# Kernel optimization log

Hardware: AMD Instinct MI355X
Metric: run time of the kernel (lower is better)

Reference implementation:

```python
import jax, jax.numpy as jnp
import numpy as np

DIM = 512
H = 8
HD = DIM // H
MAXREL = 8
BF16_MIN = -3.3895313892515355e38  # torch.finfo(torch.bfloat16).min


def setup_inputs() -> dict:
    key = jax.random.key(0)
    k1, k2, k3, k4, k5, k6 = jax.random.split(key, 6)
    b, l, n, d = 4, 16, 64, DIM
    x = jax.random.normal(k1, (b, l, n, d), dtype=jnp.float32)
    time_embeddings = jax.random.normal(k2, (b, l, d), dtype=jnp.float32)
    # relative frame positions in [-MAXREL, MAXREL]
    pos = jax.random.randint(k3, (b, l, l), 0, 2 * MAXREL + 1) - MAXREL
    pos = pos.astype(jnp.int64) if jax.config.read('jax_enable_x64') else pos.astype(jnp.int32)
    # causal mask over frames
    mask = jnp.tril(jnp.ones((l, l), dtype=jnp.int32))[None].repeat(b, axis=0)
    # params (torch Linear convention: out = x @ W.T)
    W_qkv = jax.random.normal(k4, (3 * d, d), dtype=jnp.float32) * (1.0 / np.sqrt(d))
    W_tqkv = jax.random.normal(k5, (3 * HD, d), dtype=jnp.float32) * (1.0 / np.sqrt(d))
    # xavier_uniform for embeddings table [2*max+1, head_dim]
    lim = np.sqrt(6.0 / (2 * MAXREL + 1 + HD))
    emb_table = jax.random.uniform(k6, (2 * MAXREL + 1, HD), minval=-lim, maxval=lim, dtype=jnp.float32)
    return {"x": x, "time_embeddings": time_embeddings, "pos": pos, "mask": mask,
            "W_qkv": W_qkv, "W_tqkv": W_tqkv, "emb_table": emb_table}


def _forward(x, time_embeddings, pos, mask, W_qkv, W_tqkv, emb_table):
    b, l, n, d = x.shape
    h, hd = H, HD
    N = l * n
    scale = np.sqrt(d).astype(np.float32)

    qkv = jnp.einsum('blnd,ed->blne', x, W_qkv)
    q, k, v = jnp.split(qkv, 3, axis=-1)

    def to_heads(t):  # [b,l,n,d] -> [b,h,l,n,hd]
        return t.reshape(b, l, n, h, hd).transpose(0, 3, 1, 2, 4)
    q, k, v = to_heads(q), to_heads(k), to_heads(v)

    # time qkv: [b,l,3*hd] -> broadcast add over heads and tokens
    tqkv = jnp.einsum('bld,ed->ble', time_embeddings, W_tqkv)
    qt, kt, vt = jnp.split(tqkv, 3, axis=-1)  # each [b,l,hd]

    def add_t(t, tt):  # tt: [b,l,hd] -> [b,1,l,1,hd]
        return t + tt[:, None, :, None, :]
    q = add_t(q, qt).reshape(b, h, N, hd)
    k = add_t(k, kt).reshape(b, h, N, hd)
    v = add_t(v, vt).reshape(b, h, N, hd)

    # content scores [b,h,N,N]
    qk = jnp.einsum('bhqd,bhkd->bhqk', q, k)

    # relative position bias
    idx = jnp.clip(pos, -MAXREL, MAXREL) + MAXREL          # [b,l,l]
    emb = emb_table[idx]                                    # [b,l,l,hd]
    # q chunked: [b,h,(l n),hd] -> [b,h,n,l,hd] (l is major in (l n))
    qc = q.reshape(b, h, l, n, hd).transpose(0, 1, 3, 2, 4)
    qr = jnp.einsum('bhnqd,bqkd->bhqnk', qc, emb)           # [b,h,l,n,l]
    qr = jnp.broadcast_to(qr[..., None], (b, h, l, n, l, n)).reshape(b, h, N, N)

    attn = (qk + qr) / scale

    # expand frame mask [b,l,l] -> [b,N,N]
    exp_mask = jnp.broadcast_to(mask[:, :, None, :, None], (b, l, n, l, n)).reshape(b, N, N)
    attn = jnp.where(exp_mask[:, None] == 0, BF16_MIN, attn)

    attn = jax.nn.softmax(attn, axis=-1)
    out = jnp.einsum('bhqk,bhkd->bhqd', attn, v)            # [b,h,N,hd]
    out = out.reshape(b, h, l, n, hd).transpose(0, 2, 3, 1, 4).reshape(b, l, n, d)
    return out


def reference(x, time_embeddings, pos, mask, W_qkv, W_tqkv, emb_table):
    return _forward(x, time_embeddings, pos, mask, W_qkv, W_tqkv, emb_table)
```

## Files before the change

### kernel.cpp

```cpp
#include <hip/hip_runtime.h>

typedef unsigned short u16;
typedef __attribute__((ext_vector_type(8))) short short8;
typedef __attribute__((ext_vector_type(4))) float f32x4;
typedef __attribute__((ext_vector_type(4))) u16 u16x4;

#define BB 4
#define LL 16
#define DD 512
#define NH 8
#define HDIM 64
#define NSEQ 1024
#define E3 1536
#define INV_SCALE 0.04419417382415922f

__device__ __forceinline__ u16 f2bf(float f) {
  union { float f; unsigned u; } v; v.f = f;
  unsigned u = v.u;
  unsigned r = u + 0x7fffu + ((u >> 16) & 1u);
  return (u16)(r >> 16);
}

__device__ __forceinline__ void stage16(const u16* g, u16* l) {
  __builtin_amdgcn_global_load_lds((const __attribute__((address_space(1))) unsigned int*)g,
                                   (__attribute__((address_space(3))) unsigned int*)l,
                                   16, 0, 0);
}

__global__ __launch_bounds__(256) void prep_convert(const float* __restrict__ x,
                                                    const float* __restrict__ w,
                                                    const float* __restrict__ wt,
                                                    const float* __restrict__ te,
                                                    u16* __restrict__ xbf,
                                                    u16* __restrict__ wbf,
                                                    u16* __restrict__ wtbf,
                                                    u16* __restrict__ tebf) {
  const int nx = (4096 * DD) / 4;
  const int nw = (E3 * DD) / 4;
  const int nwt = (192 * DD) / 4;
  const int nte = (64 * DD) / 4;
  int i = blockIdx.x * 256 + threadIdx.x;
  const float4* src;
  uint2* dst;
  int j;
  if (i < nx) { src = (const float4*)x; dst = (uint2*)xbf; j = i; }
  else if (i < nx + nw) { src = (const float4*)w; dst = (uint2*)wbf; j = i - nx; }
  else if (i < nx + nw + nwt) { src = (const float4*)wt; dst = (uint2*)wtbf; j = i - nx - nw; }
  else if (i < nx + nw + nwt + nte) { src = (const float4*)te; dst = (uint2*)tebf; j = i - nx - nw - nwt; }
  else return;
  float4 v = src[j];
  unsigned lo = (unsigned)f2bf(v.x) | ((unsigned)f2bf(v.y) << 16);
  unsigned hi = (unsigned)f2bf(v.z) | ((unsigned)f2bf(v.w) << 16);
  dst[j] = make_uint2(lo, hi);
}

__global__ __launch_bounds__(256) void tproj_mfma(const u16* __restrict__ tebf,
                                                  const u16* __restrict__ wtbf,
                                                  float* __restrict__ tq) {
  __shared__ u16 At[64][72];
  __shared__ u16 Bt[64][72];
  int bn = blockIdx.x;
  int tid = threadIdx.x;
  int w = tid >> 6, l = tid & 63;
  int l15 = l & 15, l16 = l >> 4;
  int r0 = tid >> 3, c0 = (tid & 7) * 8;
  f32x4 acc[4] = {};
  for (int kt = 0; kt < DD; kt += 64) {
    *(uint4*)&At[r0][c0]      = *(const uint4*)&tebf[(size_t)r0 * DD + kt + c0];
    *(uint4*)&At[r0 + 32][c0] = *(const uint4*)&tebf[(size_t)(r0 + 32) * DD + kt + c0];
    *(uint4*)&Bt[r0][c0]      = *(const uint4*)&wtbf[(size_t)(bn * 64 + r0) * DD + kt + c0];
    *(uint4*)&Bt[r0 + 32][c0] = *(const uint4*)&wtbf[(size_t)(bn * 64 + r0 + 32) * DD + kt + c0];
    __syncthreads();
#pragma unroll
    for (int ks = 0; ks < 2; ++ks) {
      short8 bfr = *(const short8*)&Bt[w * 16 + l15][ks * 32 + l16 * 8];
#pragma unroll
      for (int mt = 0; mt < 4; ++mt) {
        short8 afr = *(const short8*)&At[mt * 16 + l15][ks * 32 + l16 * 8];
        acc[mt] = __builtin_amdgcn_mfma_f32_16x16x32_bf16(afr, bfr, acc[mt], 0, 0, 0);
      }
    }
    __syncthreads();
  }
  int e = bn * 64 + w * 16 + l15;
#pragma unroll
  for (int mt = 0; mt < 4; ++mt)
#pragma unroll
    for (int r = 0; r < 4; ++r)
      tq[(mt * 16 + l16 * 4 + r) * 192 + e] = acc[mt][r];
}

__global__ __launch_bounds__(256) void gemm_qkv(const u16* __restrict__ xb,
                                                const u16* __restrict__ wb,
                                                const float* __restrict__ tq,
                                                u16* __restrict__ qp,
                                                u16* __restrict__ kp,
                                                u16* __restrict__ vt) {
  __shared__ u16 As[2][128][72];
  __shared__ u16 Bs[2][128][72];
  int bn = blockIdx.x;
  int bm = blockIdx.y;
  int tid = threadIdx.x;
  int w = tid >> 6, l = tid & 63;
  int wr = w >> 1, wc = w & 1;
  int l15 = l & 15, l16 = l >> 4;
  int r0 = tid >> 3, c0 = (tid & 7) * 8;

  f32x4 acc[4][4] = {};
  uint4 ra[4], rb[4];

#define LOADT(kt)                                                                    \
  {                                                                                  \
    _Pragma("unroll") for (int c = 0; c < 4; ++c) {                                  \
      ra[c] = *(const uint4*)&xb[(size_t)(bm * 128 + c * 32 + r0) * DD + (kt) + c0]; \
      rb[c] = *(const uint4*)&wb[(size_t)(bn * 128 + c * 32 + r0) * DD + (kt) + c0]; \
    }                                                                                \
  }
#define STORET(buf)                                                                  \
  {                                                                                  \
    _Pragma("unroll") for (int c = 0; c < 4; ++c) {                                  \
      *(uint4*)&As[buf][c * 32 + r0][c0] = ra[c];                                    \
      *(uint4*)&Bs[buf][c * 32 + r0][c0] = rb[c];                                    \
    }                                                                                \
  }

  LOADT(0);
  STORET(0);
  __syncthreads();
  int cur = 0;
#pragma unroll
  for (int i = 0; i < 8; ++i) {
    if (i < 7) LOADT((i + 1) * 64);
#pragma unroll
    for (int ks = 0; ks < 2; ++ks) {
      short8 af[4], bf[4];
#pragma unroll
      for (int mt = 0; mt < 4; ++mt)
        af[mt] = *(const short8*)&As[cur][wr * 64 + mt * 16 + l15][ks * 32 + l16 * 8];
#pragma unroll
      for (int nt = 0; nt < 4; ++nt)
        bf[nt] = *(const short8*)&Bs[cur][wc * 64 + nt * 16 + l15][ks * 32 + l16 * 8];
#pragma unroll
      for (int mt = 0; mt < 4; ++mt)
#pragma unroll
        for (int nt = 0; nt < 4; ++nt)
          acc[mt][nt] = __builtin_amdgcn_mfma_f32_16x16x32_bf16(af[mt], bf[nt], acc[mt][nt], 0, 0, 0);
    }
    if (i < 7) STORET(cur ^ 1);
    __syncthreads();
    cur ^= 1;
  }
#undef LOADT
#undef STORET

  int part = bn >> 2;
#pragma unroll
  for (int mt = 0; mt < 4; ++mt) {
    int m0 = bm * 128 + wr * 64 + mt * 16 + l16 * 4;
    int b = m0 >> 10;
    int li = (m0 >> 6) & 15;
    int nn0 = m0 & 1023;
    const float* tqrow = &tq[(b * LL + li) * 192 + part * 64];
#pragma unroll
    for (int nt = 0; nt < 4; ++nt) {
      int din = (bn & 3) * 128 + wc * 64 + nt * 16 + l15;
      int hh = din >> 6, hd = din & 63;
      float t = tqrow[hd];
      size_t bh = (size_t)(b * NH + hh);
      if (part == 2) {
        u16x4 pk;
#pragma unroll
        for (int r = 0; r < 4; ++r) pk[r] = f2bf(acc[mt][nt][r] + t);
        *(u16x4*)&vt[(bh * HDIM + hd) * NSEQ + nn0] = pk;
      } else {
        u16* dst = (part == 0) ? qp : kp;
#pragma unroll
        for (int r = 0; r < 4; ++r)
          dst[(bh * NSEQ + nn0 + r) * HDIM + hd] = f2bf(acc[mt][nt][r] + t);
      }
    }
  }
}

__global__ __launch_bounds__(256, 2) void attn_kernel(const u16* __restrict__ qp,
                                                      const u16* __restrict__ kp,
                                                      const u16* __restrict__ vt,
                                                      const int* __restrict__ pos,
                                                      const float* __restrict__ emb,
                                                      float* __restrict__ out) {
  __shared__ __align__(16) u16 Kt[2][64][64];
  __shared__ __align__(16) u16 Vt[2][64][64];
  __shared__ __align__(16) u16 Ps[4][16][64];

  int blk = blockIdx.x;
  int bhid = blk & 31;
  int qf = 15 - (blk >> 5);
  int b = bhid >> 3, h = bhid & 7;
  int tid = threadIdx.x;
  int rg = tid >> 6;
  int l = tid & 63;
  int l15 = l & 15, l16 = l >> 4;
  int srow = l >> 3, c8 = l & 7;
  int schunk = c8 ^ srow;
  int swz = (l15 & 7) << 4;

  size_t bh = (size_t)(b * NH + h);
  const u16* Kb = kp + bh * NSEQ * HDIM;
  const u16* Vb = vt + bh * HDIM * NSEQ;

  int rowl0 = rg * 16 + srow;
  int rowl1 = rowl0 + 8;

#define STAGE(kf_, buf_)                                                   \
  {                                                                        \
    stage16(Kb + ((kf_) * 64 + rowl0) * HDIM + schunk * 8,                 \
            &Kt[buf_][rg * 16 + 0][0] + l * 8);                            \
    stage16(Kb + ((kf_) * 64 + rowl1) * HDIM + schunk * 8,                 \
            &Kt[buf_][rg * 16 + 8][0] + l * 8);                            \
    stage16(Vb + (size_t)rowl0 * NSEQ + (kf_) * 64 + schunk * 8,           \
            &Vt[buf_][rg * 16 + 0][0] + l * 8);                            \
    stage16(Vb + (size_t)rowl1 * NSEQ + (kf_) * 64 + schunk * 8,           \
            &Vt[buf_][rg * 16 + 8][0] + l * 8);                            \
  }

  const u16* Qg = qp + (bh * NSEQ + qf * 64 + rg * 16) * HDIM;
  short8 aq[2];
  aq[0] = *(const short8*)&Qg[l15 * HDIM + l16 * 8];
  aq[1] = *(const short8*)&Qg[l15 * HDIM + 32 + l16 * 8];

  STAGE(0, 0);

  int pp = pos[(b * LL + qf) * LL + l15];
  pp = (pp < -8 ? -8 : (pp > 8 ? 8 : pp)) + 8;
  const float* ev = emb + pp * HDIM;
  f32x4 bfrag = {};
#pragma unroll
  for (int ks = 0; ks < 2; ++ks) {
    float4 e0 = *(const float4*)&ev[ks * 32 + l16 * 8];
    float4 e1 = *(const float4*)&ev[ks * 32 + l16 * 8 + 4];
    short8 ef;
    ef[0] = (short)f2bf(e0.x); ef[1] = (short)f2bf(e0.y);
    ef[2] = (short)f2bf(e0.z); ef[3] = (short)f2bf(e0.w);
    ef[4] = (short)f2bf(e1.x); ef[5] = (short)f2bf(e1.y);
    ef[6] = (short)f2bf(e1.z); ef[7] = (short)f2bf(e1.w);
    bfrag = __builtin_amdgcn_mfma_f32_16x16x32_bf16(aq[ks], ef, bfrag, 0, 0, 0);
  }

  f32x4 o[4] = {};
  float lsum[4] = {0.f, 0.f, 0.f, 0.f};
  const char* psb = (const char*)&Ps[rg][0][0];

  asm volatile("s_waitcnt vmcnt(0)" ::: "memory");
  __syncthreads();

  int cur = 0;
  for (int kf = 0; kf <= qf; ++kf) {
    if (kf < qf) STAGE(kf + 1, cur ^ 1);

    const char* ktb = (const char*)&Kt[cur][0][0];
    const char* vtb = (const char*)&Vt[cur][0][0];

    short8 kfrag[4][2];
#pragma unroll
    for (int nt = 0; nt < 4; ++nt)
#pragma unroll
      for (int ks = 0; ks < 2; ++ks)
        kfrag[nt][ks] = *(const short8*)(ktb + (nt * 16 + l15) * 128 + ((ks * 64 + l16 * 16) ^ swz));
    f32x4 s[4] = {};
#pragma unroll
    for (int ks = 0; ks < 2; ++ks)
#pragma unroll
      for (int nt = 0; nt < 4; ++nt)
        s[nt] = __builtin_amdgcn_mfma_f32_16x16x32_bf16(aq[ks], kfrag[nt][ks], s[nt], 0, 0, 0);

    float bb[4];
    int srcl = (l & 48) + kf;
#pragma unroll
    for (int r = 0; r < 4; ++r) bb[r] = __shfl(bfrag[r], srcl) * INV_SCALE;

#pragma unroll
    for (int nt = 0; nt < 4; ++nt)
#pragma unroll
      for (int r = 0; r < 4; ++r) {
        float p = __expf(fmaf(s[nt][r], INV_SCALE, bb[r]));
        lsum[r] += p;
        int row = l16 * 4 + r;
        *(u16*)((char*)psb + row * 128 + (((nt * 16 + l15) * 2) ^ ((row & 7) << 4))) = f2bf(p);
      }

    short8 pa[2];
#pragma unroll
    for (int ks = 0; ks < 2; ++ks)
      pa[ks] = *(const short8*)(psb + l15 * 128 + ((ks * 64 + l16 * 16) ^ swz));

    short8 vfrag[4][2];
#pragma unroll
    for (int dt = 0; dt < 4; ++dt)
#pragma unroll
      for (int ks = 0; ks < 2; ++ks)
        vfrag[dt][ks] = *(const short8*)(vtb + (dt * 16 + l15) * 128 + ((ks * 64 + l16 * 16) ^ swz));
#pragma unroll
    for (int ks = 0; ks < 2; ++ks)
#pragma unroll
      for (int dt = 0; dt < 4; ++dt)
        o[dt] = __builtin_amdgcn_mfma_f32_16x16x32_bf16(pa[ks], vfrag[dt][ks], o[dt], 0, 0, 0);

    asm volatile("s_waitcnt vmcnt(0)" ::: "memory");
    __syncthreads();
    cur ^= 1;
  }
#undef STAGE

#pragma unroll
  for (int off = 1; off < 16; off <<= 1)
#pragma unroll
    for (int r = 0; r < 4; ++r) lsum[r] += __shfl_xor(lsum[r], off);

  float* outp = out + ((size_t)(b * LL + qf) * 64 + rg * 16) * DD + h * 64;
#pragma unroll
  for (int r = 0; r < 4; ++r) {
    float inv = 1.0f / lsum[r];
#pragma unroll
    for (int dt = 0; dt < 4; ++dt)
      outp[(size_t)(l16 * 4 + r) * DD + dt * 16 + l15] = o[dt][r] * inv;
  }
}

extern "C" void kernel_launch(void* const* d_in, const int* in_sizes, int n_in,
                              void* d_out, int out_size, void* d_ws, size_t ws_size,
                              hipStream_t stream) {
  const float* x    = (const float*)d_in[0];
  const float* te   = (const float*)d_in[1];
  const int*   pos  = (const int*)d_in[2];
  const float* wqkv = (const float*)d_in[4];
  const float* wt   = (const float*)d_in[5];
  const float* emb  = (const float*)d_in[6];
  float* out = (float*)d_out;
  char* ws = (char*)d_ws;

  const size_t OFF_XBF = 0;
  const size_t OFF_WBF  = OFF_XBF + (size_t)4096 * DD * 2;
  const size_t OFF_WTBF = OFF_WBF + (size_t)E3 * DD * 2;
  const size_t OFF_TEBF = OFF_WTBF + (size_t)192 * DD * 2;
  const size_t OFF_TQ   = OFF_TEBF + (size_t)64 * DD * 2;
  const size_t OFF_QKV  = OFF_TQ + (size_t)64 * 192 * 4;
  const size_t PLANE = (size_t)BB * NH * NSEQ * HDIM;

  u16*   xbf  = (u16*)(ws + OFF_XBF);
  u16*   wbf  = (u16*)(ws + OFF_WBF);
  u16*   wtbf = (u16*)(ws + OFF_WTBF);
  u16*   tebf = (u16*)(ws + OFF_TEBF);
  float* tq   = (float*)(ws + OFF_TQ);
  u16*   qpl  = (u16*)(ws + OFF_QKV);
  u16*   kpl  = qpl + PLANE;
  u16*   vtl  = qpl + 2 * PLANE;

  prep_convert<<<2944, 256, 0, stream>>>(x, wqkv, wt, te, xbf, wbf, wtbf, tebf);
  tproj_mfma<<<3, 256, 0, stream>>>(tebf, wtbf, tq);
  gemm_qkv<<<dim3(12, 32), 256, 0, stream>>>(xbf, wbf, tq, qpl, kpl, vtl);
  attn_kernel<<<512, 256, 0, stream>>>(qpl, kpl, vtl, pos, emb, out);
}
```

Before: 118.6 us.

## Keep P in registers via transposed MFMA and deepen K/V prefetch in attention

The attention kernel now computes S transposed (K as the A operand) so each lane holds one query row's probabilities. It packs them to bf16 in registers and feeds them straight into the PV MFMA, which removes the shared-memory round trip for P. K/V staging is triple-issued, with two tiles in flight and partial vmcnt waits, and MFMA sections get s_setprio. The output goes through an LDS transpose for coalesced float4 stores, and the te/W_t bf16 conversion moves into tproj. Risks are extra LDS traffic for the output staging and split V fragment reads.

```diff
diff --git a/kernel.cpp b/kernel.cpp
--- a/kernel.cpp
+++ b/kernel.cpp
@@ -21,6 +21,21 @@
   return (u16)(r >> 16);
 }
 
+__device__ __forceinline__ unsigned cvtpk(float lo, float hi) {
+  unsigned r;
+  asm("v_cvt_pk_bf16_f32 %0, %1, %2" : "=v"(r) : "v"(lo), "v"(hi));
+  return r;
+}
+
+__device__ __forceinline__ uint4 pack8(float4 a, float4 b) {
+  uint4 r;
+  r.x = (unsigned)f2bf(a.x) | ((unsigned)f2bf(a.y) << 16);
+  r.y = (unsigned)f2bf(a.z) | ((unsigned)f2bf(a.w) << 16);
+  r.z = (unsigned)f2bf(b.x) | ((unsigned)f2bf(b.y) << 16);
+  r.w = (unsigned)f2bf(b.z) | ((unsigned)f2bf(b.w) << 16);
+  return r;
+}
+
 __device__ __forceinline__ void stage16(const u16* g, u16* l) {
   __builtin_amdgcn_global_load_lds((const __attribute__((address_space(1))) unsigned int*)g,
                                    (__attribute__((address_space(3))) unsigned int*)l,
@@ -29,24 +44,16 @@
 
 __global__ __launch_bounds__(256) void prep_convert(const float* __restrict__ x,
                                                     const float* __restrict__ w,
-                                                    const float* __restrict__ wt,
-                                                    const float* __restrict__ te,
                                                     u16* __restrict__ xbf,
-                                                    u16* __restrict__ wbf,
-                                                    u16* __restrict__ wtbf,
-                                                    u16* __restrict__ tebf) {
+                                                    u16* __restrict__ wbf) {
   const int nx = (4096 * DD) / 4;
   const int nw = (E3 * DD) / 4;
-  const int nwt = (192 * DD) / 4;
-  const int nte = (64 * DD) / 4;
   int i = blockIdx.x * 256 + threadIdx.x;
   const float4* src;
   uint2* dst;
   int j;
   if (i < nx) { src = (const float4*)x; dst = (uint2*)xbf; j = i; }
   else if (i < nx + nw) { src = (const float4*)w; dst = (uint2*)wbf; j = i - nx; }
-  else if (i < nx + nw + nwt) { src = (const float4*)wt; dst = (uint2*)wtbf; j = i - nx - nw; }
-  else if (i < nx + nw + nwt + nte) { src = (const float4*)te; dst = (uint2*)tebf; j = i - nx - nw - nwt; }
   else return;
   float4 v = src[j];
   unsigned lo = (unsigned)f2bf(v.x) | ((unsigned)f2bf(v.y) << 16);
@@ -54,8 +61,8 @@
   dst[j] = make_uint2(lo, hi);
 }
 
-__global__ __launch_bounds__(256) void tproj_mfma(const u16* __restrict__ tebf,
-                                                  const u16* __restrict__ wtbf,
+__global__ __launch_bounds__(256) void tproj_mfma(const float* __restrict__ te,
+                                                  const float* __restrict__ wt,
                                                   float* __restrict__ tq) {
   __shared__ u16 At[64][72];
   __shared__ u16 Bt[64][72];
@@ -66,10 +73,16 @@
   int r0 = tid >> 3, c0 = (tid & 7) * 8;
   f32x4 acc[4] = {};
   for (int kt = 0; kt < DD; kt += 64) {
-    *(uint4*)&At[r0][c0]      = *(const uint4*)&tebf[(size_t)r0 * DD + kt + c0];
-    *(uint4*)&At[r0 + 32][c0] = *(const uint4*)&tebf[(size_t)(r0 + 32) * DD + kt + c0];
-    *(uint4*)&Bt[r0][c0]      = *(const uint4*)&wtbf[(size_t)(bn * 64 + r0) * DD + kt + c0];
-    *(uint4*)&Bt[r0 + 32][c0] = *(const uint4*)&wtbf[(size_t)(bn * 64 + r0 + 32) * DD + kt + c0];
+    {
+      const float* ta = &te[(size_t)r0 * DD + kt + c0];
+      const float* tb = &te[(size_t)(r0 + 32) * DD + kt + c0];
+      *(uint4*)&At[r0][c0]      = pack8(*(const float4*)ta, *(const float4*)(ta + 4));
+      *(uint4*)&At[r0 + 32][c0] = pack8(*(const float4*)tb, *(const float4*)(tb + 4));
+      const float* wa = &wt[(size_t)(bn * 64 + r0) * DD + kt + c0];
+      const float* wb_ = &wt[(size_t)(bn * 64 + r0 + 32) * DD + kt + c0];
+      *(uint4*)&Bt[r0][c0]      = pack8(*(const float4*)wa, *(const float4*)(wa + 4));
+      *(uint4*)&Bt[r0 + 32][c0] = pack8(*(const float4*)wb_, *(const float4*)(wb_ + 4));
+    }
     __syncthreads();
 #pragma unroll
     for (int ks = 0; ks < 2; ++ks) {
@@ -190,7 +203,7 @@
                                                       float* __restrict__ out) {
   __shared__ __align__(16) u16 Kt[2][64][64];
   __shared__ __align__(16) u16 Vt[2][64][64];
-  __shared__ __align__(16) u16 Ps[4][16][64];
+  __shared__ __align__(16) float Ot[4][16][68];
 
   int blk = blockIdx.x;
   int bhid = blk & 31;
@@ -202,12 +215,11 @@
   int l15 = l & 15, l16 = l >> 4;
   int srow = l >> 3, c8 = l & 7;
   int schunk = c8 ^ srow;
-  int swz = (l15 & 7) << 4;
+  int swzA = (l15 & 7) << 4;
 
   size_t bh = (size_t)(b * NH + h);
   const u16* Kb = kp + bh * NSEQ * HDIM;
   const u16* Vb = vt + bh * HDIM * NSEQ;
-
   int rowl0 = rg * 16 + srow;
   int rowl1 = rowl0 + 8;
 
@@ -229,11 +241,12 @@
   aq[1] = *(const short8*)&Qg[l15 * HDIM + 32 + l16 * 8];
 
   STAGE(0, 0);
+  if (qf > 0) STAGE(1, 1);
 
   int pp = pos[(b * LL + qf) * LL + l15];
   pp = (pp < -8 ? -8 : (pp > 8 ? 8 : pp)) + 8;
   const float* ev = emb + pp * HDIM;
-  f32x4 bfrag = {};
+  f32x4 bfragT = {};
 #pragma unroll
   for (int ks = 0; ks < 2; ++ks) {
     float4 e0 = *(const float4*)&ev[ks * 32 + l16 * 8];
@@ -243,86 +256,95 @@
     ef[2] = (short)f2bf(e0.z); ef[3] = (short)f2bf(e0.w);
     ef[4] = (short)f2bf(e1.x); ef[5] = (short)f2bf(e1.y);
     ef[6] = (short)f2bf(e1.z); ef[7] = (short)f2bf(e1.w);
-    bfrag = __builtin_amdgcn_mfma_f32_16x16x32_bf16(aq[ks], ef, bfrag, 0, 0, 0);
+    bfragT = __builtin_amdgcn_mfma_f32_16x16x32_bf16(ef, aq[ks], bfragT, 0, 0, 0);
   }
 
   f32x4 o[4] = {};
-  float lsum[4] = {0.f, 0.f, 0.f, 0.f};
-  const char* psb = (const char*)&Ps[rg][0][0];
-
-  asm volatile("s_waitcnt vmcnt(0)" ::: "memory");
+  float lsum = 0.f;
+
+  if (qf > 0) { asm volatile("s_waitcnt vmcnt(4)" ::: "memory"); }
+  else        { asm volatile("s_waitcnt vmcnt(0)" ::: "memory"); }
   __syncthreads();
 
-  int cur = 0;
   for (int kf = 0; kf <= qf; ++kf) {
-    if (kf < qf) STAGE(kf + 1, cur ^ 1);
-
+    int cur = kf & 1;
     const char* ktb = (const char*)&Kt[cur][0][0];
     const char* vtb = (const char*)&Vt[cur][0][0];
 
-    short8 kfrag[4][2];
+    f32x4 s[4] = {};
+    __builtin_amdgcn_s_setprio(1);
+#pragma unroll
+    for (int ks = 0; ks < 2; ++ks)
+#pragma unroll
+      for (int nt = 0; nt < 4; ++nt) {
+        short8 kfrag = *(const short8*)(ktb + (nt * 16 + l15) * 128 + ((ks * 64 + l16 * 16) ^ swzA));
+        s[nt] = __builtin_amdgcn_mfma_f32_16x16x32_bf16(kfrag, aq[ks], s[nt], 0, 0, 0);
+      }
+    __builtin_amdgcn_s_setprio(0);
+
+    float bb = __shfl(bfragT[kf & 3], ((kf >> 2) << 4) | l15) * INV_SCALE;
+
+    float pv[4][4];
 #pragma unroll
     for (int nt = 0; nt < 4; ++nt)
 #pragma unroll
-      for (int ks = 0; ks < 2; ++ks)
-        kfrag[nt][ks] = *(const short8*)(ktb + (nt * 16 + l15) * 128 + ((ks * 64 + l16 * 16) ^ swz));
-    f32x4 s[4] = {};
-#pragma unroll
-    for (int ks = 0; ks < 2; ++ks)
-#pragma unroll
-      for (int nt = 0; nt < 4; ++nt)
-        s[nt] = __builtin_amdgcn_mfma_f32_16x16x32_bf16(aq[ks], kfrag[nt][ks], s[nt], 0, 0, 0);
-
-    float bb[4];
-    int srcl = (l & 48) + kf;
-#pragma unroll
-    for (int r = 0; r < 4; ++r) bb[r] = __shfl(bfrag[r], srcl) * INV_SCALE;
-
-#pragma unroll
-    for (int nt = 0; nt < 4; ++nt)
-#pragma unroll
       for (int r = 0; r < 4; ++r) {
-        float p = __expf(fmaf(s[nt][r], INV_SCALE, bb[r]));
-        lsum[r] += p;
-        int row = l16 * 4 + r;
-        *(u16*)((char*)psb + row * 128 + (((nt * 16 + l15) * 2) ^ ((row & 7) << 4))) = f2bf(p);
-      }
-
-    short8 pa[2];
-#pragma unroll
-    for (int ks = 0; ks < 2; ++ks)
-      pa[ks] = *(const short8*)(psb + l15 * 128 + ((ks * 64 + l16 * 16) ^ swz));
-
-    short8 vfrag[4][2];
-#pragma unroll
-    for (int dt = 0; dt < 4; ++dt)
-#pragma unroll
-      for (int ks = 0; ks < 2; ++ks)
-        vfrag[dt][ks] = *(const short8*)(vtb + (dt * 16 + l15) * 128 + ((ks * 64 + l16 * 16) ^ swz));
-#pragma unroll
-    for (int ks = 0; ks < 2; ++ks)
-#pragma unroll
-      for (int dt = 0; dt < 4; ++dt)
-        o[dt] = __builtin_amdgcn_mfma_f32_16x16x32_bf16(pa[ks], vfrag[dt][ks], o[dt], 0, 0, 0);
-
-    asm volatile("s_waitcnt vmcnt(0)" ::: "memory");
-    __syncthreads();
-    cur ^= 1;
+        float p = __expf(fmaf(s[nt][r], INV_SCALE, bb));
+        pv[nt][r] = p;
+        lsum += p;
+      }
+
+#pragma unroll
+    for (int w32 = 0; w32 < 2; ++w32) {
+      union { unsigned u[4]; short8 s8; } pf;
+      pf.u[0] = cvtpk(pv[w32 * 2][0], pv[w32 * 2][1]);
+      pf.u[1] = cvtpk(pv[w32 * 2][2], pv[w32 * 2][3]);
+      pf.u[2] = cvtpk(pv[w32 * 2 + 1][0], pv[w32 * 2 + 1][1]);
+      pf.u[3] = cvtpk(pv[w32 * 2 + 1][2], pv[w32 * 2 + 1][3]);
+      int off0 = w32 * 64 + l16 * 8;
+      int cp = off0 & ~15, sub = off0 & 15;
+      __builtin_amdgcn_s_setprio(1);
+#pragma unroll
+      for (int dt = 0; dt < 4; ++dt) {
+        int d = dt * 16 + l15;
+        int sx = (d & 7) << 4;
+        union { uint2 h2[2]; short8 s8; } vf;
+        vf.h2[0] = *(const uint2*)(vtb + d * 128 + (cp ^ sx) + sub);
+        vf.h2[1] = *(const uint2*)(vtb + d * 128 + ((cp + 32) ^ sx) + sub);
+        o[dt] = __builtin_amdgcn_mfma_f32_16x16x32_bf16(vf.s8, pf.s8, o[dt], 0, 0, 0);
+      }
+      __builtin_amdgcn_s_setprio(0);
+    }
+
+    if (kf < qf) {
+      __syncthreads();
+      if (kf + 2 <= qf) {
+        STAGE(kf + 2, cur);
+        asm volatile("s_waitcnt vmcnt(4)" ::: "memory");
+      } else {
+        asm volatile("s_waitcnt vmcnt(0)" ::: "memory");
+      }
+      __syncthreads();
+    }
   }
 #undef STAGE
 
-#pragma unroll
-  for (int off = 1; off < 16; off <<= 1)
-#pragma unroll
-    for (int r = 0; r < 4; ++r) lsum[r] += __shfl_xor(lsum[r], off);
+  lsum += __shfl_xor(lsum, 16);
+  lsum += __shfl_xor(lsum, 32);
+  float inv = 1.0f / lsum;
+
+#pragma unroll
+  for (int dt = 0; dt < 4; ++dt)
+#pragma unroll
+    for (int r = 0; r < 4; ++r)
+      Ot[rg][l15][dt * 16 + l16 * 4 + r] = o[dt][r] * inv;
 
   float* outp = out + ((size_t)(b * LL + qf) * 64 + rg * 16) * DD + h * 64;
 #pragma unroll
-  for (int r = 0; r < 4; ++r) {
-    float inv = 1.0f / lsum[r];
-#pragma unroll
-    for (int dt = 0; dt < 4; ++dt)
-      outp[(size_t)(l16 * 4 + r) * DD + dt * 16 + l15] = o[dt][r] * inv;
+  for (int rr = 0; rr < 4; ++rr) {
+    int q = rr * 4 + l16;
+    float4 v = *(const float4*)&Ot[rg][q][l15 * 4];
+    *(float4*)&outp[(size_t)q * DD + l15 * 4] = v;
   }
 }
 
@@ -340,23 +362,19 @@
 
   const size_t OFF_XBF = 0;
   const size_t OFF_WBF  = OFF_XBF + (size_t)4096 * DD * 2;
-  const size_t OFF_WTBF = OFF_WBF + (size_t)E3 * DD * 2;
-  const size_t OFF_TEBF = OFF_WTBF + (size_t)192 * DD * 2;
-  const size_t OFF_TQ   = OFF_TEBF + (size_t)64 * DD * 2;
+  const size_t OFF_TQ   = OFF_WBF + (size_t)E3 * DD * 2;
   const size_t OFF_QKV  = OFF_TQ + (size_t)64 * 192 * 4;
   const size_t PLANE = (size_t)BB * NH * NSEQ * HDIM;
 
   u16*   xbf  = (u16*)(ws + OFF_XBF);
   u16*   wbf  = (u16*)(ws + OFF_WBF);
-  u16*   wtbf = (u16*)(ws + OFF_WTBF);
-  u16*   tebf = (u16*)(ws + OFF_TEBF);
   float* tq   = (float*)(ws + OFF_TQ);
   u16*   qpl  = (u16*)(ws + OFF_QKV);
   u16*   kpl  = qpl + PLANE;
   u16*   vtl  = qpl + 2 * PLANE;
 
-  prep_convert<<<2944, 256, 0, stream>>>(x, wqkv, wt, te, xbf, wbf, wtbf, tebf);
-  tproj_mfma<<<3, 256, 0, stream>>>(tebf, wtbf, tq);
+  prep_convert<<<2816, 256, 0, stream>>>(x, wqkv, xbf, wbf);
+  tproj_mfma<<<3, 256, 0, stream>>>(te, wt, tq);
   gemm_qkv<<<dim3(12, 32), 256, 0, stream>>>(xbf, wbf, tq, qpl, kpl, vtl);
   attn_kernel<<<512, 256, 0, stream>>>(qpl, kpl, vtl, pos, emb, out);
 }
```

Measured after the change: 122.2 us. 3.1% more time.
